# Kernel tuning notes

Hardware: AMD Instinct MI355X
Metric: run time of the kernel (lower is better)

The kernel has to match this reference:

```python
import jax, jax.numpy as jnp
import numpy as np

B = 8          # number of subgraphs (seq_start_end rows)
N = 2048       # nodes per subgraph (equal-size segments)
D = 64         # h_dim
H = 4          # gat_heads
ALPHA = 0.2    # leaky relu slope


def setup_inputs() -> dict:
    key = jax.random.key(0)
    k1, k2, k3, k4, k5 = jax.random.split(key, 5)
    h_states = jax.random.normal(k1, (B * N, D), dtype=jnp.float32)
    # xavier-ish scales
    W_heads = jax.random.normal(k2, (H, D, D), dtype=jnp.float32) * (1.414 * np.sqrt(2.0 / (D + D)))
    a_heads = jax.random.normal(k3, (H, 2 * D), dtype=jnp.float32) * (1.414 * np.sqrt(2.0 / (2 * D + 1)))
    W_out = jax.random.normal(k4, (H * D, D), dtype=jnp.float32) * (1.414 * np.sqrt(2.0 / (H * D + D)))
    a_out = jax.random.normal(k5, (2 * D,), dtype=jnp.float32) * (1.414 * np.sqrt(2.0 / (2 * D + 1)))
    starts = jnp.arange(B, dtype=jnp.int32) * N
    seq_start_end = jnp.stack([starts, starts + N], axis=1)  # (B, 2)
    return {"h_states": h_states, "W_heads": W_heads, "a_heads": a_heads,
            "W_out": W_out, "a_out": a_out, "seq_start_end": seq_start_end}


def _gat_layer(x, W, a):
    """Dense GAT layer. Equivalent to the torch.cat O(N^2*2d) construction,
    rewritten as separate a1/a2 projections + broadcast add. Eval mode (no dropout)."""
    h = x @ W                      # (N, dout)
    d = W.shape[1]
    s1 = h @ a[:d]                 # (N,)  score contribution of source node i
    s2 = h @ a[d:]                 # (N,)  score contribution of target node j
    e = jax.nn.leaky_relu(s1[:, None] + s2[None, :], ALPHA)  # (N, N)
    attn = jax.nn.softmax(e, axis=1)
    return attn @ h                # (N, dout)


def reference(h_states, W_heads, a_heads, W_out, a_out, seq_start_end):
    # seq_start_end encodes B equal contiguous segments of length N -> reshape
    x = h_states.reshape(B, N, D)

    def per_graph(xg):  # xg: (N, D)
        # multi-head attention layers, concat=True -> elu on each head output
        hp = jax.vmap(lambda W, a: jax.nn.elu(_gat_layer(xg, W, a)))(W_heads, a_heads)  # (H, N, D)
        xc = jnp.transpose(hp, (1, 0, 2)).reshape(N, H * D)
        # output attention layer, concat=False (no elu inside), then elu + log_softmax outside
        out = jax.nn.elu(_gat_layer(xc, W_out, a_out))   # (N, D)
        return jax.nn.log_softmax(out, axis=1)

    return jax.vmap(per_graph)(x).reshape(B * N, D)
```

## Files before the change

### kernel.cpp

```cpp
#include <hip/hip_runtime.h>
#include <math.h>

#define NTOT 16384
#define NSEG 2048
#define TROW 65
#define TSTRIDE 133185ull

#define OFF_HH   0ull
#define OFF_XC   4194304ull
#define OFF_S1H  8388608ull
#define OFF_S2H  8454144ull
#define OFF_S1O  8519680ull
#define OFF_S2O  8536064ull
#define OFF_SVAL 8552448ull
#define OFF_WN   8617984ull
#define OFF_CHA  8683520ull
#define OFF_CHS  8949760ull
#define OFF_SIDX 9216000ull
#define OFF_A    9281536ull
#define OFF_S    13543456ull

__device__ inline unsigned long long pack_key(float v, int idx) {
    unsigned u = __float_as_uint(v);
    u = (u & 0x80000000u) ? ~u : (u | 0x80000000u);
    return ((unsigned long long)u << 32) | (unsigned)idx;
}
__device__ inline float unpack_key(unsigned long long k) {
    unsigned u = (unsigned)(k >> 32);
    u = (u & 0x80000000u) ? (u ^ 0x80000000u) : ~u;
    return __uint_as_float(u);
}
__device__ inline unsigned long long shfl_xor_u64(unsigned long long x, int mask) {
    unsigned lo = (unsigned)x, hi = (unsigned)(x >> 32);
    lo = (unsigned)__shfl_xor((int)lo, mask, 64);
    hi = (unsigned)__shfl_xor((int)hi, mask, 64);
    return ((unsigned long long)hi << 32) | lo;
}

__global__ __launch_bounds__(256) void gemm1_k(const float* __restrict__ X,
                                               const float* __restrict__ Wh,
                                               const float* __restrict__ aH,
                                               float* __restrict__ hh,
                                               float* __restrict__ s1h,
                                               float* __restrict__ s2h) {
    __shared__ float As[64][68];
    __shared__ float Bs[64][68];
    const int tid = threadIdx.x;
    const int bm = blockIdx.x, h = blockIdx.y;
    const int c0 = tid & 63, r0 = tid >> 6;
#pragma unroll
    for (int r = 0; r < 16; ++r) {
        int row = r0 + r * 4;
        As[c0][row] = X[(size_t)(bm * 64 + row) * 64 + c0];
        Bs[row][c0] = Wh[h * 4096 + row * 64 + c0];
    }
    __syncthreads();
    const int tx = tid & 15, ty = tid >> 4;
    const int m0 = ty * 4, n0 = tx * 4;
    float acc[4][4] = {};
#pragma unroll
    for (int kk = 0; kk < 64; ++kk) {
        float4 a = *(const float4*)&As[kk][m0];
        float4 b = *(const float4*)&Bs[kk][n0];
        acc[0][0] += a.x * b.x; acc[0][1] += a.x * b.y; acc[0][2] += a.x * b.z; acc[0][3] += a.x * b.w;
        acc[1][0] += a.y * b.x; acc[1][1] += a.y * b.y; acc[1][2] += a.y * b.z; acc[1][3] += a.y * b.w;
        acc[2][0] += a.z * b.x; acc[2][1] += a.z * b.y; acc[2][2] += a.z * b.z; acc[2][3] += a.z * b.w;
        acc[3][0] += a.w * b.x; acc[3][1] += a.w * b.y; acc[3][2] += a.w * b.z; acc[3][3] += a.w * b.w;
    }
#pragma unroll
    for (int i = 0; i < 4; ++i) {
        float4 v = make_float4(acc[i][0], acc[i][1], acc[i][2], acc[i][3]);
        *(float4*)&hh[(size_t)(bm * 64 + m0 + i) * 256 + h * 64 + n0] = v;
    }
#pragma unroll
    for (int i = 0; i < 4; ++i) {
        float p1 = 0.f, p2 = 0.f;
#pragma unroll
        for (int jj = 0; jj < 4; ++jj) {
            p1 += acc[i][jj] * aH[h * 128 + n0 + jj];
            p2 += acc[i][jj] * aH[h * 128 + 64 + n0 + jj];
        }
#pragma unroll
        for (int off = 8; off; off >>= 1) {
            p1 += __shfl_xor(p1, off, 16);
            p2 += __shfl_xor(p2, off, 16);
        }
        if (tx == 0) {
            s1h[h * NTOT + bm * 64 + m0 + i] = p1;
            s2h[h * NTOT + bm * 64 + m0 + i] = p2;
        }
    }
}

__global__ __launch_bounds__(256) void gemm2_k(const float* __restrict__ XC,
                                               const float* __restrict__ Wo,
                                               const float* __restrict__ aO,
                                               float* __restrict__ hc,
                                               float* __restrict__ s1o,
                                               float* __restrict__ s2o) {
    __shared__ float As[64][68];
    __shared__ float Bs[64][68];
    const int tid = threadIdx.x;
    const int bm = blockIdx.x;
    const int c0 = tid & 63, r0 = tid >> 6;
    const int tx = tid & 15, ty = tid >> 4;
    const int m0 = ty * 4, n0 = tx * 4;
    float acc[4][4] = {};
    for (int kt = 0; kt < 4; ++kt) {
#pragma unroll
        for (int r = 0; r < 16; ++r) {
            int row = r0 + r * 4;
            As[c0][row] = XC[(size_t)(bm * 64 + row) * 256 + kt * 64 + c0];
            Bs[row][c0] = Wo[(kt * 64 + row) * 64 + c0];
        }
        __syncthreads();
#pragma unroll
        for (int kk = 0; kk < 64; ++kk) {
            float4 a = *(const float4*)&As[kk][m0];
            float4 b = *(const float4*)&Bs[kk][n0];
            acc[0][0] += a.x * b.x; acc[0][1] += a.x * b.y; acc[0][2] += a.x * b.z; acc[0][3] += a.x * b.w;
            acc[1][0] += a.y * b.x; acc[1][1] += a.y * b.y; acc[1][2] += a.y * b.z; acc[1][3] += a.y * b.w;
            acc[2][0] += a.z * b.x; acc[2][1] += a.z * b.y; acc[2][2] += a.z * b.z; acc[2][3] += a.z * b.w;
            acc[3][0] += a.w * b.x; acc[3][1] += a.w * b.y; acc[3][2] += a.w * b.z; acc[3][3] += a.w * b.w;
        }
        __syncthreads();
    }
#pragma unroll
    for (int i = 0; i < 4; ++i) {
        float4 v = make_float4(acc[i][0], acc[i][1], acc[i][2], acc[i][3]);
        *(float4*)&hc[(size_t)(bm * 64 + m0 + i) * 64 + n0] = v;
    }
#pragma unroll
    for (int i = 0; i < 4; ++i) {
        float p1 = 0.f, p2 = 0.f;
#pragma unroll
        for (int jj = 0; jj < 4; ++jj) {
            p1 += acc[i][jj] * aO[n0 + jj];
            p2 += acc[i][jj] * aO[64 + n0 + jj];
        }
#pragma unroll
        for (int off = 8; off; off >>= 1) {
            p1 += __shfl_xor(p1, off, 16);
            p2 += __shfl_xor(p2, off, 16);
        }
        if (tx == 0) {
            s1o[bm * 64 + m0 + i] = p1;
            s2o[bm * 64 + m0 + i] = p2;
        }
    }
}

__global__ __launch_bounds__(1024) void sortchunkscan_k(const float* __restrict__ s2_all,
                                                        const float* __restrict__ V,
                                                        int heads, int vstride,
                                                        float* __restrict__ g_sval, int* __restrict__ g_sidx,
                                                        float* __restrict__ g_wN,
                                                        float* __restrict__ g_chA, float* __restrict__ g_chS,
                                                        float* __restrict__ g_A, float* __restrict__ g_S) {
    __shared__ unsigned long long sA[1024];
    __shared__ unsigned long long sB[1024];
    __shared__ float chA[8320];
    __shared__ float chS[8320];
    __shared__ float swn[NSEG];
    __shared__ int ssi[NSEG];
    __shared__ float btA[4][65];
    __shared__ float btS[4][65];
    __shared__ float sM2;
    const int tid = threadIdx.x, t = blockIdx.x;
    const int g = t / heads, h = t % heads;
    const float* s2p = s2_all + (size_t)h * NTOT + (size_t)g * NSEG;
    const float* Vp = V + (size_t)g * NSEG * vstride + h * 64;

    unsigned long long a0 = pack_key(s2p[tid], tid);
    unsigned long long a1 = pack_key(s2p[tid + 1024], tid + 1024);
    for (int k = 2; k <= 2048; k <<= 1) {
        const bool up0 = (tid & k) == 0;
        const bool up1 = (((tid + 1024) & k) == 0);
        for (int j = k >> 1; j > 0; j >>= 1) {
            if (j >= 1024) {
                unsigned long long lo = a0 < a1 ? a0 : a1;
                unsigned long long hi = a0 < a1 ? a1 : a0;
                a0 = up0 ? lo : hi;
                a1 = up0 ? hi : lo;
            } else if (j >= 64) {
                __syncthreads();
                sA[tid] = a0; sB[tid] = a1;
                __syncthreads();
                unsigned long long p0 = sA[tid ^ j], p1 = sB[tid ^ j];
                bool lower = (tid & j) == 0;
                a0 = ((a0 < p0) == (lower == up0)) ? a0 : p0;
                a1 = ((a1 < p1) == (lower == up1)) ? a1 : p1;
            } else {
                unsigned long long p0 = shfl_xor_u64(a0, j);
                unsigned long long p1 = shfl_xor_u64(a1, j);
                bool lower = (tid & j) == 0;
                a0 = ((a0 < p0) == (lower == up0)) ? a0 : p0;
                a1 = ((a1 < p1) == (lower == up1)) ? a1 : p1;
            }
        }
    }
    float v0 = unpack_key(a0), v1 = unpack_key(a1);
    if (tid == 1023) sM2 = v1;
    __syncthreads();
    const float M2 = sM2;
    int i0 = (int)(unsigned)(a0 & 0xffffffffu);
    int i1 = (int)(unsigned)(a1 & 0xffffffffu);
    float w0 = __expf(0.2f * (v0 - M2));
    float w1 = __expf(0.2f * (v1 - M2));
    size_t o = (size_t)t * NSEG;
    g_sval[o + tid] = v0; g_sval[o + tid + 1024] = v1;
    g_sidx[o + tid] = i0; g_sidx[o + tid + 1024] = i1;
    g_wN[o + tid] = w0;   g_wN[o + tid + 1024] = w1;
    swn[tid] = w0; swn[tid + 1024] = w1;
    ssi[tid] = i0; ssi[tid + 1024] = i1;
    __syncthreads();
    const int wv = tid >> 6, lane = tid & 63;
    for (int cc = 0; cc < 8; ++cc) {
        int c = wv * 8 + cc, base = c * 16;
        float sa = 0.f, swa = 0.f, ss = 0.f, sws = 0.f;
#pragma unroll
        for (int j = 0; j < 16; ++j) {
            float wn = swn[base + j];
            int row = ssi[base + j];
            float v = Vp[(size_t)row * vstride + lane];
            float w2 = wn * wn, wp = w2 * w2 * wn;
            sa += wn * v; swa += wn;
            ss += wp * v; sws += wp;
        }
        chA[c * 65 + lane] = sa; chS[c * 65 + lane] = ss;
        if (lane == 0) { chA[c * 65 + 64] = swa; chS[c * 65 + 64] = sws; }
    }
    __syncthreads();
    if (tid < 260) {
        int b = tid / 65, d = tid % 65;
        float run = 0.f;
        for (int c = b * 32; c < b * 32 + 32; ++c) { float v = chA[c * 65 + d]; chA[c * 65 + d] = run; run += v; }
        btA[b][d] = run;
    } else if (tid >= 512 && tid < 772) {
        int u = tid - 512;
        int b = u / 65, d = u % 65;
        float run = 0.f;
        for (int c = b * 32 + 31; c >= b * 32; --c) { run += chS[c * 65 + d]; chS[c * 65 + d] = run; }
        btS[b][d] = run;
    }
    __syncthreads();
    if (tid < 65) {
        float run = 0.f;
        for (int b = 0; b < 4; ++b) { float v = btA[b][tid]; btA[b][tid] = run; run += v; }
        g_A[(size_t)t * TSTRIDE + (size_t)2048 * TROW + tid] = run;
    } else if (tid >= 512 && tid < 577) {
        int d = tid - 512;
        float run = 0.f;
        for (int b = 3; b >= 0; --b) { float v = btS[b][d]; btS[b][d] = run; run += v; }
        g_S[(size_t)t * TSTRIDE + (size_t)2048 * TROW + d] = 0.f;
    }
    __syncthreads();
    if (tid < 512) {
        for (int i = tid; i < 8320; i += 512) chA[i] += btA[(i / 65) >> 5][i % 65];
    } else {
        for (int i = tid - 512; i < 8320; i += 512) chS[i] += btS[(i / 65) >> 5][i % 65];
    }
    __syncthreads();
    for (int i = tid; i < 8320; i += 1024) {
        g_chA[(size_t)t * 8320 + i] = chA[i];
        g_chS[(size_t)t * 8320 + i] = chS[i];
    }
}

__global__ __launch_bounds__(256) void seg_tab_k(const float* __restrict__ V,
                                                 int heads, int vstride,
                                                 const int* __restrict__ g_sidx,
                                                 const float* __restrict__ g_wN,
                                                 const float* __restrict__ g_chA,
                                                 const float* __restrict__ g_chS,
                                                 float* __restrict__ g_A, float* __restrict__ g_S) {
    const int t = blockIdx.y, g = t / heads, h = t % heads;
    const int wv = threadIdx.x >> 6, lane = threadIdx.x & 63;
    const int c = blockIdx.x * 4 + wv;
    const int base = c * 16;
    const float* Vp = V + (size_t)g * NSEG * vstride + h * 64;
    const int* sidx = g_sidx + (size_t)t * NSEG + base;
    const float* wnp = g_wN + (size_t)t * NSEG + base;
    float wn[16], vv[16];
#pragma unroll
    for (int j = 0; j < 16; ++j) wn[j] = wnp[j];
#pragma unroll
    for (int j = 0; j < 16; ++j) vv[j] = Vp[(size_t)sidx[j] * vstride + lane];
    float* A = g_A + (size_t)t * TSTRIDE;
    float* S = g_S + (size_t)t * TSTRIDE;
    float accA = g_chA[((size_t)t * 128 + c) * TROW + lane];
    float scaA = g_chA[((size_t)t * 128 + c) * TROW + 64];
#pragma unroll
    for (int j = 0; j < 16; ++j) {
        size_t pos = base + j;
        A[pos * TROW + lane] = accA;
        if (lane == 0) A[pos * TROW + 64] = scaA;
        accA += wn[j] * vv[j]; scaA += wn[j];
    }
    float accS = 0.f, scaS = 0.f;
    if (c < 127) {
        accS = g_chS[((size_t)t * 128 + c + 1) * TROW + lane];
        scaS = g_chS[((size_t)t * 128 + c + 1) * TROW + 64];
    }
#pragma unroll
    for (int j = 15; j >= 0; --j) {
        float w = wn[j], w2 = w * w, wp = w2 * w2 * w;
        accS += wp * vv[j]; scaS += wp;
        size_t pos = base + j;
        S[pos * TROW + lane] = accS;
        if (lane == 0) S[pos * TROW + 64] = scaS;
    }
}

template <int MODE>
__global__ __launch_bounds__(256) void seg_query_k(const float* __restrict__ s1_all,
                                                   float* __restrict__ out,
                                                   int heads, int ostride,
                                                   const float* __restrict__ g_sval,
                                                   const float* __restrict__ g_A,
                                                   const float* __restrict__ g_S) {
    __shared__ float sval[NSEG];
    const int tid = threadIdx.x;
    const int t = blockIdx.y, g = t / heads, h = t % heads;
    const float4* sv4 = (const float4*)(g_sval + (size_t)t * NSEG);
    for (int i = tid; i < NSEG / 4; i += 256) ((float4*)sval)[i] = sv4[i];
    __syncthreads();
    const float M2 = sval[NSEG - 1];
    const int lane = tid & 63, wv = tid >> 6;
    const int q0 = blockIdx.x * 64 + wv * 16;
    const float* s1p = s1_all + (size_t)h * NTOT + (size_t)g * NSEG;
    float* outp = out + (size_t)g * NSEG * ostride + h * 64;
    const float* A = g_A + (size_t)t * TSTRIDE;
    const float* S = g_S + (size_t)t * TSTRIDE;
    int myq = q0 + (lane & 15);
    float s1v = s1p[myq];
    float th = -s1v;
    int lo = 0, hi = NSEG;
    while (lo < hi) { int mid = (lo + hi) >> 1; if (sval[mid] <= th) lo = mid + 1; else hi = mid; }
    for (int j = 0; j < 16; ++j) {
        int k = __shfl(lo, j, 64);
        float s1q = __shfl(s1v, j, 64);
        const float* rowA = A + (size_t)k * TROW;
        const float* rowS = S + (size_t)k * TROW;
        float accA = rowA[lane], scaA = rowA[64];
        float accS = rowS[lane], scaS = rowS[64];
        float cc = __expf(-0.8f * fmaxf(s1q + M2, 0.f));
        float o = (accS + cc * accA) / (scaS + cc * scaA);
        o = o > 0.f ? o : expm1f(o);
        int q = q0 + j;
        if (MODE == 0) {
            outp[(size_t)q * ostride + lane] = o;
        } else {
            float m = o;
#pragma unroll
            for (int off = 32; off; off >>= 1) m = fmaxf(m, __shfl_xor(m, off, 64));
            float e = __expf(o - m);
#pragma unroll
            for (int off = 32; off; off >>= 1) e += __shfl_xor(e, off, 64);
            outp[(size_t)q * ostride + lane] = o - m - __logf(e);
        }
    }
}

extern "C" void kernel_launch(void* const* d_in, const int* in_sizes, int n_in,
                              void* d_out, int out_size, void* d_ws, size_t ws_size,
                              hipStream_t stream) {
    const float* h_states = (const float*)d_in[0];
    const float* W_heads = (const float*)d_in[1];
    const float* a_heads = (const float*)d_in[2];
    const float* W_out = (const float*)d_in[3];
    const float* a_out = (const float*)d_in[4];
    float* w = (float*)d_ws;
    float* hh = w + OFF_HH;
    float* xc = w + OFF_XC;
    float* hc = w + OFF_HH;
    float* s1h = w + OFF_S1H;
    float* s2h = w + OFF_S2H;
    float* s1o = w + OFF_S1O;
    float* s2o = w + OFF_S2O;
    float* g_sval = w + OFF_SVAL;
    float* g_wN = w + OFF_WN;
    float* g_chA = w + OFF_CHA;
    float* g_chS = w + OFF_CHS;
    int* g_sidx = (int*)(w + OFF_SIDX);
    float* g_A = w + OFF_A;
    float* g_S = w + OFF_S;
    float* outp = (float*)d_out;

    gemm1_k<<<dim3(256, 4), 256, 0, stream>>>(h_states, W_heads, a_heads, hh, s1h, s2h);
    sortchunkscan_k<<<32, 1024, 0, stream>>>(s2h, hh, 4, 256, g_sval, g_sidx, g_wN, g_chA, g_chS, g_A, g_S);
    seg_tab_k<<<dim3(32, 32), 256, 0, stream>>>(hh, 4, 256, g_sidx, g_wN, g_chA, g_chS, g_A, g_S);
    seg_query_k<0><<<dim3(32, 32), 256, 0, stream>>>(s1h, xc, 4, 256, g_sval, g_A, g_S);
    gemm2_k<<<256, 256, 0, stream>>>(xc, W_out, a_out, hc, s1o, s2o);
    sortchunkscan_k<<<8, 1024, 0, stream>>>(s2o, hc, 1, 64, g_sval, g_sidx, g_wN, g_chA, g_chS, g_A, g_S);
    seg_tab_k<<<dim3(32, 8), 256, 0, stream>>>(hc, 1, 64, g_sidx, g_wN, g_chA, g_chS, g_A, g_S);
    seg_query_k<1><<<dim3(32, 8), 256, 0, stream>>>(s1o, outp, 1, 64, g_sval, g_A, g_S);
}
```

Measured before the change: 203.7 us.

## Replace per-position prefix tables with chunk prefixes plus in-query chunk reconstruction

Removes the seg_tab kernel, which materialized full per-position prefix/suffix tables (2048x65 floats each, per head and graph). The sort kernel now also writes a sorted copy of V. Each query loads the chunk-level prefix and suffix rows and recomputes the partial sums over the 16 elements of its chunk. This cuts a kernel launch and a large amount of global writes and reads, at the cost of 16 extra sorted-V loads and some arithmetic per query row.

```diff
diff --git a/kernel.cpp b/kernel.cpp
--- a/kernel.cpp
+++ b/kernel.cpp
@@ -3,8 +3,7 @@
 
 #define NTOT 16384
 #define NSEG 2048
-#define TROW 65
-#define TSTRIDE 133185ull
+#define CROWS 8385ull
 
 #define OFF_HH   0ull
 #define OFF_XC   4194304ull
@@ -15,10 +14,8 @@
 #define OFF_SVAL 8552448ull
 #define OFF_WN   8617984ull
 #define OFF_CHA  8683520ull
-#define OFF_CHS  8949760ull
-#define OFF_SIDX 9216000ull
-#define OFF_A    9281536ull
-#define OFF_S    13543456ull
+#define OFF_CHS  8951840ull
+#define OFF_VS   9220160ull
 
 __device__ inline unsigned long long pack_key(float v, int idx) {
     unsigned u = __float_as_uint(v);
@@ -153,10 +150,10 @@
 __global__ __launch_bounds__(1024) void sortchunkscan_k(const float* __restrict__ s2_all,
                                                         const float* __restrict__ V,
                                                         int heads, int vstride,
-                                                        float* __restrict__ g_sval, int* __restrict__ g_sidx,
+                                                        float* __restrict__ g_sval,
                                                         float* __restrict__ g_wN,
                                                         float* __restrict__ g_chA, float* __restrict__ g_chS,
-                                                        float* __restrict__ g_A, float* __restrict__ g_S) {
+                                                        float* __restrict__ g_Vs) {
     __shared__ unsigned long long sA[1024];
     __shared__ unsigned long long sB[1024];
     __shared__ float chA[8320];
@@ -170,6 +167,7 @@
     const int g = t / heads, h = t % heads;
     const float* s2p = s2_all + (size_t)h * NTOT + (size_t)g * NSEG;
     const float* Vp = V + (size_t)g * NSEG * vstride + h * 64;
+    float* Vst = g_Vs + (size_t)t * NSEG * 64;
 
     unsigned long long a0 = pack_key(s2p[tid], tid);
     unsigned long long a1 = pack_key(s2p[tid + 1024], tid + 1024);
@@ -209,7 +207,6 @@
     float w1 = __expf(0.2f * (v1 - M2));
     size_t o = (size_t)t * NSEG;
     g_sval[o + tid] = v0; g_sval[o + tid + 1024] = v1;
-    g_sidx[o + tid] = i0; g_sidx[o + tid + 1024] = i1;
     g_wN[o + tid] = w0;   g_wN[o + tid + 1024] = w1;
     swn[tid] = w0; swn[tid + 1024] = w1;
     ssi[tid] = i0; ssi[tid + 1024] = i1;
@@ -223,6 +220,7 @@
             float wn = swn[base + j];
             int row = ssi[base + j];
             float v = Vp[(size_t)row * vstride + lane];
+            Vst[(size_t)(base + j) * 64 + lane] = v;
             float w2 = wn * wn, wp = w2 * w2 * wn;
             sa += wn * v; swa += wn;
             ss += wp * v; sws += wp;
@@ -247,12 +245,12 @@
     if (tid < 65) {
         float run = 0.f;
         for (int b = 0; b < 4; ++b) { float v = btA[b][tid]; btA[b][tid] = run; run += v; }
-        g_A[(size_t)t * TSTRIDE + (size_t)2048 * TROW + tid] = run;
+        g_chA[(size_t)t * CROWS + 8320 + tid] = run;
     } else if (tid >= 512 && tid < 577) {
         int d = tid - 512;
         float run = 0.f;
         for (int b = 3; b >= 0; --b) { float v = btS[b][d]; btS[b][d] = run; run += v; }
-        g_S[(size_t)t * TSTRIDE + (size_t)2048 * TROW + d] = 0.f;
+        g_chS[(size_t)t * CROWS + 8320 + d] = 0.f;
     }
     __syncthreads();
     if (tid < 512) {
@@ -262,53 +260,8 @@
     }
     __syncthreads();
     for (int i = tid; i < 8320; i += 1024) {
-        g_chA[(size_t)t * 8320 + i] = chA[i];
-        g_chS[(size_t)t * 8320 + i] = chS[i];
-    }
-}
-
-__global__ __launch_bounds__(256) void seg_tab_k(const float* __restrict__ V,
-                                                 int heads, int vstride,
-                                                 const int* __restrict__ g_sidx,
-                                                 const float* __restrict__ g_wN,
-                                                 const float* __restrict__ g_chA,
-                                                 const float* __restrict__ g_chS,
-                                                 float* __restrict__ g_A, float* __restrict__ g_S) {
-    const int t = blockIdx.y, g = t / heads, h = t % heads;
-    const int wv = threadIdx.x >> 6, lane = threadIdx.x & 63;
-    const int c = blockIdx.x * 4 + wv;
-    const int base = c * 16;
-    const float* Vp = V + (size_t)g * NSEG * vstride + h * 64;
-    const int* sidx = g_sidx + (size_t)t * NSEG + base;
-    const float* wnp = g_wN + (size_t)t * NSEG + base;
-    float wn[16], vv[16];
-#pragma unroll
-    for (int j = 0; j < 16; ++j) wn[j] = wnp[j];
-#pragma unroll
-    for (int j = 0; j < 16; ++j) vv[j] = Vp[(size_t)sidx[j] * vstride + lane];
-    float* A = g_A + (size_t)t * TSTRIDE;
-    float* S = g_S + (size_t)t * TSTRIDE;
-    float accA = g_chA[((size_t)t * 128 + c) * TROW + lane];
-    float scaA = g_chA[((size_t)t * 128 + c) * TROW + 64];
-#pragma unroll
-    for (int j = 0; j < 16; ++j) {
-        size_t pos = base + j;
-        A[pos * TROW + lane] = accA;
-        if (lane == 0) A[pos * TROW + 64] = scaA;
-        accA += wn[j] * vv[j]; scaA += wn[j];
-    }
-    float accS = 0.f, scaS = 0.f;
-    if (c < 127) {
-        accS = g_chS[((size_t)t * 128 + c + 1) * TROW + lane];
-        scaS = g_chS[((size_t)t * 128 + c + 1) * TROW + 64];
-    }
-#pragma unroll
-    for (int j = 15; j >= 0; --j) {
-        float w = wn[j], w2 = w * w, wp = w2 * w2 * w;
-        accS += wp * vv[j]; scaS += wp;
-        size_t pos = base + j;
-        S[pos * TROW + lane] = accS;
-        if (lane == 0) S[pos * TROW + 64] = scaS;
+        g_chA[(size_t)t * CROWS + i] = chA[i];
+        g_chS[(size_t)t * CROWS + i] = chS[i];
     }
 }
 
@@ -317,21 +270,29 @@
                                                    float* __restrict__ out,
                                                    int heads, int ostride,
                                                    const float* __restrict__ g_sval,
-                                                   const float* __restrict__ g_A,
-                                                   const float* __restrict__ g_S) {
+                                                   const float* __restrict__ g_wN,
+                                                   const float* __restrict__ g_chA,
+                                                   const float* __restrict__ g_chS,
+                                                   const float* __restrict__ g_Vs) {
     __shared__ float sval[NSEG];
+    __shared__ float swn[NSEG];
     const int tid = threadIdx.x;
     const int t = blockIdx.y, g = t / heads, h = t % heads;
     const float4* sv4 = (const float4*)(g_sval + (size_t)t * NSEG);
-    for (int i = tid; i < NSEG / 4; i += 256) ((float4*)sval)[i] = sv4[i];
+    const float4* wn4 = (const float4*)(g_wN + (size_t)t * NSEG);
+    for (int i = tid; i < NSEG / 4; i += 256) {
+        ((float4*)sval)[i] = sv4[i];
+        ((float4*)swn)[i] = wn4[i];
+    }
     __syncthreads();
     const float M2 = sval[NSEG - 1];
     const int lane = tid & 63, wv = tid >> 6;
     const int q0 = blockIdx.x * 64 + wv * 16;
     const float* s1p = s1_all + (size_t)h * NTOT + (size_t)g * NSEG;
     float* outp = out + (size_t)g * NSEG * ostride + h * 64;
-    const float* A = g_A + (size_t)t * TSTRIDE;
-    const float* S = g_S + (size_t)t * TSTRIDE;
+    const float* cAg = g_chA + (size_t)t * CROWS;
+    const float* cSg = g_chS + (size_t)t * CROWS;
+    const float* Vst = g_Vs + (size_t)t * NSEG * 64;
     int myq = q0 + (lane & 15);
     float s1v = s1p[myq];
     float th = -s1v;
@@ -340,10 +301,22 @@
     for (int j = 0; j < 16; ++j) {
         int k = __shfl(lo, j, 64);
         float s1q = __shfl(s1v, j, 64);
-        const float* rowA = A + (size_t)k * TROW;
-        const float* rowS = S + (size_t)k * TROW;
-        float accA = rowA[lane], scaA = rowA[64];
-        float accS = rowS[lane], scaS = rowS[64];
+        int ck = k >> 4; if (ck > 127) ck = 127;
+        const float* rA = cAg + ck * 65;
+        const float* rS = cSg + (ck + 1) * 65;
+        float accA = rA[lane], scaA = rA[64];
+        float accS = rS[lane], scaS = rS[64];
+        int base = ck * 16;
+#pragma unroll
+        for (int jj = 0; jj < 16; ++jj) {
+            int pos = base + jj;
+            float v = Vst[(size_t)pos * 64 + lane];
+            float wn = swn[pos];
+            float w2 = wn * wn, wp = w2 * w2 * wn;
+            bool isA = pos < k;
+            accA += isA ? wn * v : 0.f; scaA += isA ? wn : 0.f;
+            accS += isA ? 0.f : wp * v; scaS += isA ? 0.f : wp;
+        }
         float cc = __expf(-0.8f * fmaxf(s1q + M2, 0.f));
         float o = (accS + cc * accA) / (scaS + cc * scaA);
         o = o > 0.f ? o : expm1f(o);
@@ -382,17 +355,13 @@
     float* g_wN = w + OFF_WN;
     float* g_chA = w + OFF_CHA;
     float* g_chS = w + OFF_CHS;
-    int* g_sidx = (int*)(w + OFF_SIDX);
-    float* g_A = w + OFF_A;
-    float* g_S = w + OFF_S;
+    float* g_Vs = w + OFF_VS;
     float* outp = (float*)d_out;
 
     gemm1_k<<<dim3(256, 4), 256, 0, stream>>>(h_states, W_heads, a_heads, hh, s1h, s2h);
-    sortchunkscan_k<<<32, 1024, 0, stream>>>(s2h, hh, 4, 256, g_sval, g_sidx, g_wN, g_chA, g_chS, g_A, g_S);
-    seg_tab_k<<<dim3(32, 32), 256, 0, stream>>>(hh, 4, 256, g_sidx, g_wN, g_chA, g_chS, g_A, g_S);
-    seg_query_k<0><<<dim3(32, 32), 256, 0, stream>>>(s1h, xc, 4, 256, g_sval, g_A, g_S);
+    sortchunkscan_k<<<32, 1024, 0, stream>>>(s2h, hh, 4, 256, g_sval, g_wN, g_chA, g_chS, g_Vs);
+    seg_query_k<0><<<dim3(32, 32), 256, 0, stream>>>(s1h, xc, 4, 256, g_sval, g_wN, g_chA, g_chS, g_Vs);
     gemm2_k<<<256, 256, 0, stream>>>(xc, W_out, a_out, hc, s1o, s2o);
-    sortchunkscan_k<<<8, 1024, 0, stream>>>(s2o, hc, 1, 64, g_sval, g_sidx, g_wN, g_chA, g_chS, g_A, g_S);
-    seg_tab_k<<<dim3(32, 8), 256, 0, stream>>>(hc, 1, 64, g_sidx, g_wN, g_chA, g_chS, g_A, g_S);
-    seg_query_k<1><<<dim3(32, 8), 256, 0, stream>>>(s1o, outp, 1, 64, g_sval, g_A, g_S);
-}
+    sortchunkscan_k<<<8, 1024, 0, stream>>>(s2o, hc, 1, 64, g_sval, g_wN, g_chA, g_chS, g_Vs);
+    seg_query_k<1><<<dim3(32, 8), 256, 0, stream>>>(s1o, outp, 1, 64, g_sval, g_wN, g_chA, g_chS, g_Vs);
+}
```

Result: slower. 228.0 us (+11.9%).
